# Kernel optimization log

Measured on AMD Instinct MI355X. Metric: run time of the kernel, lower is better.

## Reference

```python
import jax, jax.numpy as jnp
import numpy as np
from jax import lax

EPS = 1e-5

def _conv3x3(x, w, stride=1):
    # x: [B,C,H,W], w: [O,I,3,3]
    dn = lax.conv_dimension_numbers(x.shape, w.shape, ('NCHW', 'OIHW', 'NCHW'))
    return lax.conv_general_dilated(x, w, window_strides=(stride, stride),
                                    padding=((1, 1), (1, 1)), dimension_numbers=dn)

def _batchnorm(x, gamma, beta):
    # training-mode BN over (N,H,W) per channel
    mean = jnp.mean(x, axis=(0, 2, 3), keepdims=True)
    var = jnp.var(x, axis=(0, 2, 3), keepdims=True)
    inv = lax.rsqrt(var + EPS)
    return (x - mean) * inv * gamma[None, :, None, None] + beta[None, :, None, None]

def setup_inputs() -> dict:
    key = jax.random.key(0)
    ks = jax.random.split(key, 8)
    B, C, H, W, E = 16, 256, 64, 64, 512
    x = jax.random.normal(ks[0], (B, C, H, W), dtype=jnp.float32)
    embedding = jax.random.normal(ks[1], (B, E), dtype=jnp.float32)
    s_conv = 1.0 / np.sqrt(C * 9)
    conv1_w = jax.random.normal(ks[2], (C, C, 3, 3), dtype=jnp.float32) * s_conv
    conv2_w = jax.random.normal(ks[3], (C, C, 3, 3), dtype=jnp.float32) * s_conv
    s_g = 1.0 / np.sqrt(E)
    g1_w = jax.random.normal(ks[4], (E, C), dtype=jnp.float32) * s_g
    g1_b = jnp.zeros((C,), dtype=jnp.float32)
    g2_w = jax.random.normal(ks[5], (E, C), dtype=jnp.float32) * s_g
    g2_b = jnp.zeros((C,), dtype=jnp.float32)
    bn1_g = jnp.ones((C,), dtype=jnp.float32)
    bn1_b = jnp.zeros((C,), dtype=jnp.float32)
    bn2_g = jnp.ones((C,), dtype=jnp.float32)
    bn2_b = jnp.zeros((C,), dtype=jnp.float32)
    return {"x": x, "embedding": embedding, "conv1_w": conv1_w, "conv2_w": conv2_w,
            "g1_w": g1_w, "g1_b": g1_b, "g2_w": g2_w, "g2_b": g2_b,
            "bn1_g": bn1_g, "bn1_b": bn1_b, "bn2_g": bn2_g, "bn2_b": bn2_b}

def reference(x, embedding, conv1_w, conv2_w, g1_w, g1_b, g2_w, g2_b,
              bn1_g, bn1_b, bn2_g, bn2_b):
    identity = x
    # gate 1: per-sample per-channel gate values (softmax over channels)
    gate1 = jax.nn.softmax(embedding @ g1_w + g1_b, axis=-1)  # [B,C]
    out = _conv3x3(x, conv1_w, stride=1) * gate1[:, :, None, None]
    out = jax.nn.relu(_batchnorm(out, bn1_g, bn1_b))
    # gate 2
    gate2 = jax.nn.softmax(embedding @ g2_w + g2_b, axis=-1)  # [B,C]
    out = _conv3x3(out, conv2_w, stride=1) * gate2[:, :, None, None]
    out = _batchnorm(out, bn2_g, bn2_b)
    out = jax.nn.relu(out + identity)
    return (out, gate1, gate2)
```

## Files before the change

### kernel.cpp

```cpp
#include <hip/hip_runtime.h>

typedef __attribute__((ext_vector_type(8))) short short8;
typedef __attribute__((ext_vector_type(4))) float f32x4;

#define HP 66

__device__ __forceinline__ unsigned short f2bf(float f) {
  unsigned u = __builtin_bit_cast(unsigned, f);
  u += 0x7FFFu + ((u >> 16) & 1u);
  return (unsigned short)(u >> 16);
}
__device__ __forceinline__ float bf2f(unsigned short h) {
  return __builtin_bit_cast(float, ((unsigned)h) << 16);
}
__device__ __forceinline__ __attribute__((address_space(3))) void* to_as3(void* p) {
  return (__attribute__((address_space(3))) void*)(unsigned)(unsigned long long)p;
}
__device__ __forceinline__ const __attribute__((address_space(1))) void* to_as1(const void* p) {
  return (const __attribute__((address_space(1))) void*)(unsigned long long)p;
}

#define SB0() __builtin_amdgcn_sched_barrier(0)
#define BAR() do { SB0(); __builtin_amdgcn_s_barrier(); SB0(); } while (0)

__global__ void k_halo_zero(unsigned int* xp) {
  int p = blockIdx.x % 260;
  int b = blockIdx.x / 260;
  int h, w;
  if (p < 66)      { h = 0;  w = p; }
  else if (p < 132){ h = 65; w = p - 66; }
  else             { int q = p - 132; h = 1 + (q >> 1); w = (q & 1) * 65; }
  unsigned int* dst = xp + ((long)((b*HP + h)*HP + w) * 256) / 2;
  dst[threadIdx.x] = 0u;
  dst[threadIdx.x + 64] = 0u;
}

__global__ __launch_bounds__(256) void k_convert_x(const float* __restrict__ x,
                                                   unsigned short* __restrict__ xp) {
  __shared__ float tile[32][65];
  int blk = blockIdx.x;
  int ct = blk & 7, h = (blk >> 3) & 63, b = blk >> 9;
  int c0 = ct * 32;
  int t = threadIdx.x;
  int w = t & 63, cs = t >> 6;
#pragma unroll
  for (int i = 0; i < 8; ++i) {
    int c = cs + i * 4;
    tile[c][w] = x[(((b * 256) + c0 + c) * 64 + h) * 64 + w];
  }
  __syncthreads();
  int cl = (t & 15) * 2, w0 = t >> 4;
#pragma unroll
  for (int i = 0; i < 4; ++i) {
    int ww = w0 + i * 16;
    unsigned v = (unsigned)f2bf(tile[cl][ww]) | ((unsigned)f2bf(tile[cl + 1][ww]) << 16);
    *(unsigned*)(xp + ((long)((b*HP + h + 1)*HP + (ww + 1)) * 256 + c0 + cl)) = v;
  }
}

__global__ void k_pack_w(const float* __restrict__ w1, const float* __restrict__ w2,
                         unsigned short* __restrict__ wT1, unsigned short* __restrict__ wT2) {
  const float* w = blockIdx.y ? w2 : w1;
  unsigned short* wT = blockIdx.y ? wT2 : wT1;
  int co = blockIdx.x;
  int t = threadIdx.x;
#pragma unroll
  for (int kk = 0; kk < 9; ++kk) {
    wT[co * 2304 + kk * 256 + t] = f2bf(w[(co * 256 + t) * 9 + kk]);
  }
}

__global__ __launch_bounds__(256) void k_gates(const float* __restrict__ emb,
                                               const float* __restrict__ g1w,
                                               const float* __restrict__ g1b,
                                               const float* __restrict__ g2w,
                                               const float* __restrict__ g2b,
                                               float* __restrict__ gate1,
                                               float* __restrict__ gate2) {
  const float* gw = blockIdx.y ? g2w : g1w;
  const float* gbias = blockIdx.y ? g2b : g1b;
  float* gout = blockIdx.y ? gate2 : gate1;
  __shared__ float ebuf[512];
  __shared__ float red[8];
  int b = blockIdx.x, t = threadIdx.x;
  ebuf[t] = emb[b * 512 + t];
  ebuf[t + 256] = emb[b * 512 + t + 256];
  __syncthreads();
  float acc = gbias[t];
  for (int k = 0; k < 512; ++k) acc += ebuf[k] * gw[k * 256 + t];
  float mx = acc;
  for (int off = 32; off >= 1; off >>= 1) mx = fmaxf(mx, __shfl_xor(mx, off));
  if ((t & 63) == 0) red[t >> 6] = mx;
  __syncthreads();
  mx = fmaxf(fmaxf(red[0], red[1]), fmaxf(red[2], red[3]));
  float e = expf(acc - mx);
  float sm = e;
  for (int off = 32; off >= 1; off >>= 1) sm += __shfl_xor(sm, off);
  if ((t & 63) == 0) red[4 + (t >> 6)] = sm;
  __syncthreads();
  sm = red[4] + red[5] + red[6] + red[7];
  gout[b * 256 + t] = e / sm;
}

__global__ __launch_bounds__(512, 2) void k_conv(
    const unsigned short* __restrict__ inp,
    const unsigned short* __restrict__ wT,
    const float* __restrict__ gate,
    unsigned short* __restrict__ yout,
    float* __restrict__ partials) {
  __shared__ short As[2][256][64];
  __shared__ short Bs[2][256][64];
  __shared__ float sbuf[2][256][2];

  const int t = threadIdx.x;
  const int lane = t & 63;
  const int wid = t >> 6;
  const int wm = wid >> 2;
  const int wn = wid & 3;
  const int lr = lane & 15;
  const int hi = lane >> 4;
  const int key = lr & 7;

  const int blk = ((blockIdx.x & 7) << 5) + (blockIdx.x >> 3);
  const int b = blk >> 4;
  const int hh4 = (blk & 15) << 2;

  const int r0 = t >> 3;
  const int cdst = (t & 7) << 3;
  const int cg8 = (((t & 7) ^ ((t >> 3) & 7)) << 3);

  int aoff[4];
#pragma unroll
  for (int i = 0; i < 4; ++i)
    aoff[i] = (b * HP + hh4 + i) * HP + r0;

  auto stageA = [&](int buf, int half, int s) {
    int kk = s >> 2;
    int kh = (kk * 11) >> 5;
    int khw = kh * 66 + (kk - kh * 3);
    int ci = ((s & 3) << 6) + cg8;
    const unsigned short* g0 = inp + (long)(aoff[half * 2 + 0] + khw) * 256 + ci;
    const unsigned short* g1 = inp + (long)(aoff[half * 2 + 1] + khw) * 256 + ci;
    __builtin_amdgcn_global_load_lds(to_as1(g0), to_as3((void*)&As[buf][half * 128 + r0][cdst]), 16, 0, 0);
    __builtin_amdgcn_global_load_lds(to_as1(g1), to_as3((void*)&As[buf][half * 128 + 64 + r0][cdst]), 16, 0, 0);
  };
  auto stageB = [&](int buf, int half, int s) {
    int co0 = half * 128 + r0;
    const unsigned short* g0 = wT + (long)co0 * 2304 + s * 64 + cg8;
    const unsigned short* g1 = wT + (long)(co0 + 64) * 2304 + s * 64 + cg8;
    __builtin_amdgcn_global_load_lds(to_as1(g0), to_as3((void*)&Bs[buf][half * 128 + r0][cdst]), 16, 0, 0);
    __builtin_amdgcn_global_load_lds(to_as1(g1), to_as3((void*)&Bs[buf][half * 128 + 64 + r0][cdst]), 16, 0, 0);
  };

  f32x4 acc[8][4];
#pragma unroll
  for (int i = 0; i < 8; ++i)
#pragma unroll
    for (int j = 0; j < 4; ++j) acc[i][j] = (f32x4){0.f, 0.f, 0.f, 0.f};

  short8 afrag0[4][2], afrag1[4][2];
  short8 bfrag0[2][2], bfrag1[2][2];

#define RD_A(ARR, MH, BUF)                                                           \
  _Pragma("unroll") for (int mf = 0; mf < 4; ++mf)                                   \
    _Pragma("unroll") for (int ks = 0; ks < 2; ++ks)                                 \
      ARR[mf][ks] = *(const short8*)&As[BUF][wm * 128 + ((MH) * 4 + mf) * 16 + lr][((ks * 4 + hi) ^ key) << 3];
#define RD_B(ARR, NH, BUF)                                                           \
  _Pragma("unroll") for (int nf = 0; nf < 2; ++nf)                                   \
    _Pragma("unroll") for (int ks = 0; ks < 2; ++ks)                                 \
      ARR[nf][ks] = *(const short8*)&Bs[BUF][wn * 64 + ((NH) * 2 + nf) * 16 + lr][((ks * 4 + hi) ^ key) << 3];

#define QUADQ(AF, BF, mh, nh)                                                        \
  do {                                                                               \
    __builtin_amdgcn_s_setprio(1);                                                   \
    _Pragma("unroll") for (int ks = 0; ks < 2; ++ks)                                 \
      _Pragma("unroll") for (int mo = 0; mo < 4; ++mo)                               \
        _Pragma("unroll") for (int no = 0; no < 2; ++no)                             \
          acc[(mh) * 4 + mo][(nh) * 2 + no] = __builtin_amdgcn_mfma_f32_16x16x32_bf16( \
              AF[mo][ks], BF[no][ks], acc[(mh) * 4 + mo][(nh) * 2 + no], 0, 0, 0);   \
    __builtin_amdgcn_s_setprio(0);                                                   \
  } while (0)

  stageB(0, 1, 0); stageA(0, 0, 0); stageB(0, 0, 0); stageA(0, 1, 0);
  stageB(1, 1, 1); stageA(1, 0, 1); stageB(1, 0, 1); stageA(1, 1, 1);
  asm volatile("s_waitcnt vmcnt(8)" ::: "memory");
  BAR();
  RD_B(bfrag0, 0, 0);
  RD_A(afrag0, 0, 0);

#define KTHALF2(SEL, kt)                                                             \
  {                                                                                  \
    RD_B(bfrag1, 1, SEL);                                                            \
    RD_A(afrag1, 1, SEL);                                                            \
    if ((kt) + 2 < 36) stageB(SEL, 1, (kt) + 2);                                     \
    SB0();                                                                           \
    QUADQ(afrag0, bfrag0, 0, 0);                                                     \
    QUADQ(afrag0, bfrag1, 0, 1);                                                     \
    QUADQ(afrag1, bfrag0, 1, 0);                                                     \
    if ((kt) < 34) { asm volatile("s_waitcnt vmcnt(4)" ::: "memory"); }              \
    else           { asm volatile("s_waitcnt vmcnt(2)" ::: "memory"); }              \
    BAR();                                                                           \
    if ((kt) < 35) { RD_B(bfrag0, 0, SEL ^ 1); RD_A(afrag0, 0, SEL ^ 1); }           \
    if ((kt) + 2 < 36) { stageA(SEL, 0, (kt) + 2); stageB(SEL, 0, (kt) + 2); stageA(SEL, 1, (kt) + 2); } \
    SB0();                                                                           \
    QUADQ(afrag1, bfrag1, 1, 1);                                                     \
    if ((kt) < 34) { asm volatile("s_waitcnt vmcnt(8)" ::: "memory"); }              \
    else           { asm volatile("s_waitcnt vmcnt(0)" ::: "memory"); }              \
    BAR();                                                                           \
  }

  for (int i = 0; i < 18; ++i) {
    const int kt0 = 2 * i;
    KTHALF2(0, kt0)
    KTHALF2(1, kt0 + 1)
  }
#undef KTHALF2
#undef QUADQ
#undef RD_A
#undef RD_B

  float g[4];
#pragma unroll
  for (int nf = 0; nf < 4; ++nf) g[nf] = gate[(b << 8) + wn * 64 + nf * 16 + lr];

  float s[4] = {0, 0, 0, 0}, sq[4] = {0, 0, 0, 0};
  const int mrow0 = (blk << 8) + wm * 128 + (hi << 2);
  const int c0 = wn * 64 + lr;
#pragma unroll
  for (int mf = 0; mf < 8; ++mf)
#pragma unroll
    for (int r = 0; r < 4; ++r) {
      const int mm = mrow0 + mf * 16 + r;
#pragma unroll
      for (int nf = 0; nf < 4; ++nf) {
        float v = acc[mf][nf][r] * g[nf];
        yout[(long)mm * 256 + c0 + nf * 16] = f2bf(v);
        s[nf] += v;
        sq[nf] += v * v;
      }
    }
#pragma unroll
  for (int nf = 0; nf < 4; ++nf) {
    s[nf] += __shfl_xor(s[nf], 16);  s[nf] += __shfl_xor(s[nf], 32);
    sq[nf] += __shfl_xor(sq[nf], 16); sq[nf] += __shfl_xor(sq[nf], 32);
  }
  if (hi == 0) {
#pragma unroll
    for (int nf = 0; nf < 4; ++nf) {
      int c = wn * 64 + nf * 16 + lr;
      sbuf[wm][c][0] = s[nf];
      sbuf[wm][c][1] = sq[nf];
    }
  }
  __syncthreads();
  if (t < 256) {
    partials[((blk << 8) + t) * 2]     = sbuf[0][t][0] + sbuf[1][t][0];
    partials[((blk << 8) + t) * 2 + 1] = sbuf[0][t][1] + sbuf[1][t][1];
  }
}

__global__ __launch_bounds__(256) void k_bnfin(const float* __restrict__ partials,
                                               const float* __restrict__ gamma,
                                               const float* __restrict__ beta,
                                               float2* __restrict__ aff) {
  __shared__ float red[8];
  int c = blockIdx.x, t = threadIdx.x;
  float s = partials[(t * 256 + c) * 2];
  float sq = partials[(t * 256 + c) * 2 + 1];
  for (int off = 32; off >= 1; off >>= 1) { s += __shfl_xor(s, off); sq += __shfl_xor(sq, off); }
  if ((t & 63) == 0) { red[t >> 6] = s; red[4 + (t >> 6)] = sq; }
  __syncthreads();
  if (t == 0) {
    s = red[0] + red[1] + red[2] + red[3];
    sq = red[4] + red[5] + red[6] + red[7];
    float mean = s * (1.0f / 65536.0f);
    float var = fmaxf(sq * (1.0f / 65536.0f) - mean * mean, 0.0f);
    float inv = rsqrtf(var + 1e-5f);
    float ga = gamma[c] * inv;
    aff[c] = make_float2(ga, beta[c] - mean * ga);
  }
}

__global__ __launch_bounds__(256) void k_mid(const unsigned short* __restrict__ y1,
                                             const float2* __restrict__ aff,
                                             unsigned short* __restrict__ zp) {
  long idx = (long)blockIdx.x * 256 + threadIdx.x;
  int c0 = (int)(idx & 31) * 8;
  long pos = idx >> 5;
  int b = (int)(pos >> 12), hw = (int)(pos & 4095);
  int h = hw >> 6, w = hw & 63;
  uint4 v = *(const uint4*)(y1 + pos * 256 + c0);
  unsigned vv[4] = {v.x, v.y, v.z, v.w};
  unsigned outp[4];
#pragma unroll
  for (int j = 0; j < 4; ++j) {
    float2 aL = aff[c0 + 2 * j], aH = aff[c0 + 2 * j + 1];
    float lo = fmaxf(aL.x * bf2f((unsigned short)(vv[j] & 0xFFFF)) + aL.y, 0.f);
    float hiv = fmaxf(aH.x * bf2f((unsigned short)(vv[j] >> 16)) + aH.y, 0.f);
    outp[j] = (unsigned)f2bf(lo) | ((unsigned)f2bf(hiv) << 16);
  }
  unsigned short* dst = zp + (long)((b * HP + h + 1) * HP + w + 1) * 256 + c0;
  *(uint4*)dst = make_uint4(outp[0], outp[1], outp[2], outp[3]);
}

__global__ __launch_bounds__(256) void k_final(const unsigned short* __restrict__ y2,
                                               const float2* __restrict__ aff,
                                               const float* __restrict__ x,
                                               float* __restrict__ out) {
  __shared__ float tile[64][33];
  int blk = blockIdx.x;
  int ct = blk & 7, h = (blk >> 3) & 63, b = blk >> 9;
  int c0 = ct * 32;
  int t = threadIdx.x;
  int cl = (t & 15) * 2, w0 = t >> 4;
#pragma unroll
  for (int i = 0; i < 4; ++i) {
    int w = w0 + i * 16;
    unsigned v = *(const unsigned*)(y2 + (long)((b * 4096) + h * 64 + w) * 256 + c0 + cl);
    float2 aL = aff[c0 + cl], aH = aff[c0 + cl + 1];
    tile[w][cl] = aL.x * bf2f((unsigned short)(v & 0xFFFF)) + aL.y;
    tile[w][cl + 1] = aH.x * bf2f((unsigned short)(v >> 16)) + aH.y;
  }
  __syncthreads();
  int w = t & 63, csub = t >> 6;
#pragma unroll
  for (int j = 0; j < 8; ++j) {
    int c = c0 + csub * 8 + j;
    long o = ((long)(b * 256 + c) * 64 + h) * 64 + w;
    out[o] = fmaxf(tile[w][csub * 8 + j] + x[o], 0.f);
  }
}

extern "C" void kernel_launch(void* const* d_in, const int* in_sizes, int n_in,
                              void* d_out, int out_size, void* d_ws, size_t ws_size,
                              hipStream_t stream) {
  const float* x    = (const float*)d_in[0];
  const float* emb  = (const float*)d_in[1];
  const float* w1   = (const float*)d_in[2];
  const float* w2   = (const float*)d_in[3];
  const float* g1w  = (const float*)d_in[4];
  const float* g1b  = (const float*)d_in[5];
  const float* g2w  = (const float*)d_in[6];
  const float* g2b  = (const float*)d_in[7];
  const float* bn1g = (const float*)d_in[8];
  const float* bn1b = (const float*)d_in[9];
  const float* bn2g = (const float*)d_in[10];
  const float* bn2b = (const float*)d_in[11];

  float* out = (float*)d_out;
  float* gate1 = out + 16777216;
  float* gate2 = gate1 + 4096;

  char* ws = (char*)d_ws;
  const size_t OFF_XP  = 0;
  const size_t OFF_WT1 = 35684352;
  const size_t OFF_WT2 = OFF_WT1 + 1179648;
  const size_t OFF_Y   = OFF_WT2 + 1179648;
  const size_t OFF_PART = OFF_Y + 33554432;
  const size_t OFF_AFF1 = OFF_PART + 1048576;
  const size_t OFF_AFF2 = OFF_AFF1 + 2048;

  unsigned short* xp  = (unsigned short*)(ws + OFF_XP);
  unsigned short* wT1 = (unsigned short*)(ws + OFF_WT1);
  unsigned short* wT2 = (unsigned short*)(ws + OFF_WT2);
  unsigned short* y   = (unsigned short*)(ws + OFF_Y);
  float* part = (float*)(ws + OFF_PART);
  float2* aff1 = (float2*)(ws + OFF_AFF1);
  float2* aff2 = (float2*)(ws + OFF_AFF2);

  k_halo_zero<<<16 * 260, 64, 0, stream>>>((unsigned int*)xp);
  k_convert_x<<<8192, 256, 0, stream>>>(x, xp);
  k_pack_w<<<dim3(256, 2), 256, 0, stream>>>(w1, w2, wT1, wT2);
  k_gates<<<dim3(16, 2), 256, 0, stream>>>(emb, g1w, g1b, g2w, g2b, gate1, gate2);

  k_conv<<<256, 512, 0, stream>>>(xp, wT1, gate1, y, part);
  k_bnfin<<<256, 256, 0, stream>>>(part, bn1g, bn1b, aff1);
  k_mid<<<8192, 256, 0, stream>>>(y, aff1, xp);

  k_conv<<<256, 512, 0, stream>>>(xp, wT2, gate2, y, part);
  k_bnfin<<<256, 256, 0, stream>>>(part, bn2g, bn2b, aff2);
  k_final<<<8192, 256, 0, stream>>>(y, aff2, x, out);
}
```

Measured before the change: 226.5 us.

## Load conv weight fragments directly from global into registers, dropping LDS B staging

The weight operand B is no longer staged through shared memory. Each lane now loads its MFMA B fragments straight from global memory into double-buffered registers one k-step ahead, while only the activation tile A goes through LDS. This halves LDS footprint and removes the B LDS reads and writes. It also rewrites the pipeline schedule and waitcnt counts. The cost is more VGPR pressure and redundant global/L2 weight reads across the two wm warps, plus exposed global latency if the prefetch distance is too short.

```diff
diff --git a/kernel.cpp b/kernel.cpp
--- a/kernel.cpp
+++ b/kernel.cpp
@@ -109,7 +109,6 @@
     unsigned short* __restrict__ yout,
     float* __restrict__ partials) {
   __shared__ short As[2][256][64];
-  __shared__ short Bs[2][256][64];
   __shared__ float sbuf[2][256][2];
 
   const int t = threadIdx.x;
@@ -144,13 +143,8 @@
     __builtin_amdgcn_global_load_lds(to_as1(g0), to_as3((void*)&As[buf][half * 128 + r0][cdst]), 16, 0, 0);
     __builtin_amdgcn_global_load_lds(to_as1(g1), to_as3((void*)&As[buf][half * 128 + 64 + r0][cdst]), 16, 0, 0);
   };
-  auto stageB = [&](int buf, int half, int s) {
-    int co0 = half * 128 + r0;
-    const unsigned short* g0 = wT + (long)co0 * 2304 + s * 64 + cg8;
-    const unsigned short* g1 = wT + (long)(co0 + 64) * 2304 + s * 64 + cg8;
-    __builtin_amdgcn_global_load_lds(to_as1(g0), to_as3((void*)&Bs[buf][half * 128 + r0][cdst]), 16, 0, 0);
-    __builtin_amdgcn_global_load_lds(to_as1(g1), to_as3((void*)&Bs[buf][half * 128 + 64 + r0][cdst]), 16, 0, 0);
-  };
+
+  const unsigned short* wTq = wT + (long)(wn * 64 + lr) * 2304 + hi * 8;
 
   f32x4 acc[8][4];
 #pragma unroll
@@ -158,66 +152,85 @@
 #pragma unroll
     for (int j = 0; j < 4; ++j) acc[i][j] = (f32x4){0.f, 0.f, 0.f, 0.f};
 
-  short8 afrag0[4][2], afrag1[4][2];
-  short8 bfrag0[2][2], bfrag1[2][2];
-
-#define RD_A(ARR, MH, BUF)                                                           \
+  short8 afrag[4][2];
+  short8 bfA[4][2], bfB[4][2];
+
+#define LD_B(BF, kt)                                                                 \
+  _Pragma("unroll") for (int nf = 0; nf < 4; ++nf)                                   \
+    _Pragma("unroll") for (int ks = 0; ks < 2; ++ks)                                 \
+      BF[nf][ks] = *(const short8*)(wTq + (long)nf * 16 * 2304 + (kt) * 64 + ks * 32);
+
+#define RD_A(MH, BUF)                                                                \
   _Pragma("unroll") for (int mf = 0; mf < 4; ++mf)                                   \
     _Pragma("unroll") for (int ks = 0; ks < 2; ++ks)                                 \
-      ARR[mf][ks] = *(const short8*)&As[BUF][wm * 128 + ((MH) * 4 + mf) * 16 + lr][((ks * 4 + hi) ^ key) << 3];
-#define RD_B(ARR, NH, BUF)                                                           \
-  _Pragma("unroll") for (int nf = 0; nf < 2; ++nf)                                   \
-    _Pragma("unroll") for (int ks = 0; ks < 2; ++ks)                                 \
-      ARR[nf][ks] = *(const short8*)&Bs[BUF][wn * 64 + ((NH) * 2 + nf) * 16 + lr][((ks * 4 + hi) ^ key) << 3];
-
-#define QUADQ(AF, BF, mh, nh)                                                        \
+      afrag[mf][ks] = *(const short8*)&As[BUF][wm * 128 + ((MH) * 4 + mf) * 16 + lr][((ks * 4 + hi) ^ key) << 3];
+
+#define QUADN(BF, mh, nh)                                                            \
   do {                                                                               \
     __builtin_amdgcn_s_setprio(1);                                                   \
     _Pragma("unroll") for (int ks = 0; ks < 2; ++ks)                                 \
       _Pragma("unroll") for (int mo = 0; mo < 4; ++mo)                               \
         _Pragma("unroll") for (int no = 0; no < 2; ++no)                             \
           acc[(mh) * 4 + mo][(nh) * 2 + no] = __builtin_amdgcn_mfma_f32_16x16x32_bf16( \
-              AF[mo][ks], BF[no][ks], acc[(mh) * 4 + mo][(nh) * 2 + no], 0, 0, 0);   \
+              afrag[mo][ks], BF[(nh) * 2 + no][ks],                                  \
+              acc[(mh) * 4 + mo][(nh) * 2 + no], 0, 0, 0);                           \
     __builtin_amdgcn_s_setprio(0);                                                   \
   } while (0)
 
-  stageB(0, 1, 0); stageA(0, 0, 0); stageB(0, 0, 0); stageA(0, 1, 0);
-  stageB(1, 1, 1); stageA(1, 0, 1); stageB(1, 0, 1); stageA(1, 1, 1);
-  asm volatile("s_waitcnt vmcnt(8)" ::: "memory");
+  stageA(0, 0, 0); stageA(0, 1, 0);
+  stageA(1, 0, 1); stageA(1, 1, 1);
+  LD_B(bfA, 0);
+  asm volatile("s_waitcnt vmcnt(0)" ::: "memory");
   BAR();
-  RD_B(bfrag0, 0, 0);
-  RD_A(afrag0, 0, 0);
-
-#define KTHALF2(SEL, kt)                                                             \
+  RD_A(0, 0);
+
+#define KT_STEADY(SEL, kt, BC, BN_)                                                  \
   {                                                                                  \
-    RD_B(bfrag1, 1, SEL);                                                            \
-    RD_A(afrag1, 1, SEL);                                                            \
-    if ((kt) + 2 < 36) stageB(SEL, 1, (kt) + 2);                                     \
+    LD_B(BN_, (kt) + 1);                                                             \
     SB0();                                                                           \
-    QUADQ(afrag0, bfrag0, 0, 0);                                                     \
-    QUADQ(afrag0, bfrag1, 0, 1);                                                     \
-    QUADQ(afrag1, bfrag0, 1, 0);                                                     \
-    if ((kt) < 34) { asm volatile("s_waitcnt vmcnt(4)" ::: "memory"); }              \
-    else           { asm volatile("s_waitcnt vmcnt(2)" ::: "memory"); }              \
+    QUADN(BC, 0, 0);                                                                 \
+    QUADN(BC, 0, 1);                                                                 \
+    RD_A(1, SEL);                                                                    \
+    QUADN(BC, 1, 0);                                                                 \
+    QUADN(BC, 1, 1);                                                                 \
     BAR();                                                                           \
-    if ((kt) < 35) { RD_B(bfrag0, 0, SEL ^ 1); RD_A(afrag0, 0, SEL ^ 1); }           \
-    if ((kt) + 2 < 36) { stageA(SEL, 0, (kt) + 2); stageB(SEL, 0, (kt) + 2); stageA(SEL, 1, (kt) + 2); } \
-    SB0();                                                                           \
-    QUADQ(afrag1, bfrag1, 1, 1);                                                     \
-    if ((kt) < 34) { asm volatile("s_waitcnt vmcnt(8)" ::: "memory"); }              \
-    else           { asm volatile("s_waitcnt vmcnt(0)" ::: "memory"); }              \
+    stageA(SEL, 0, (kt) + 2); stageA(SEL, 1, (kt) + 2);                              \
+    asm volatile("s_waitcnt vmcnt(12)" ::: "memory");                                \
+    RD_A(0, SEL ^ 1);                                                                \
+    asm volatile("s_waitcnt vmcnt(4)" ::: "memory");                                 \
     BAR();                                                                           \
   }
 
-  for (int i = 0; i < 18; ++i) {
+  for (int i = 0; i < 17; ++i) {
     const int kt0 = 2 * i;
-    KTHALF2(0, kt0)
-    KTHALF2(1, kt0 + 1)
-  }
-#undef KTHALF2
-#undef QUADQ
+    KT_STEADY(0, kt0, bfA, bfB)
+    KT_STEADY(1, kt0 + 1, bfB, bfA)
+  }
+  {
+    LD_B(bfB, 35);
+    SB0();
+    QUADN(bfA, 0, 0);
+    QUADN(bfA, 0, 1);
+    RD_A(1, 0);
+    QUADN(bfA, 1, 0);
+    QUADN(bfA, 1, 1);
+    BAR();
+    asm volatile("s_waitcnt vmcnt(8)" ::: "memory");
+    RD_A(0, 1);
+    asm volatile("s_waitcnt vmcnt(0)" ::: "memory");
+    BAR();
+  }
+  {
+    QUADN(bfB, 0, 0);
+    QUADN(bfB, 0, 1);
+    RD_A(1, 1);
+    QUADN(bfB, 1, 0);
+    QUADN(bfB, 1, 1);
+  }
+#undef KT_STEADY
+#undef QUADN
 #undef RD_A
-#undef RD_B
+#undef LD_B
 
   float g[4];
 #pragma unroll
@@ -244,6 +257,7 @@
     s[nf] += __shfl_xor(s[nf], 16);  s[nf] += __shfl_xor(s[nf], 32);
     sq[nf] += __shfl_xor(sq[nf], 16); sq[nf] += __shfl_xor(sq[nf], 32);
   }
+  __syncthreads();
   if (hi == 0) {
 #pragma unroll
     for (int nf = 0; nf < 4; ++nf) {
```

New measurement: 293.0 us. 29.3% more time.

## Merge prep kernels into one launch and stage conv output through LDS

Applied to the files above, without the earlier changes.

Folds the halo-zero, input conversion, weight packing and gate softmax kernels into one k_prep launch that dispatches on block index, cutting three kernel launches and their gaps. In the conv epilogue, the gated bf16 results are first written into the reused LDS pool and then stored to global memory as coalesced 16-byte rows, replacing scattered 2-byte stores. LDS is now a single aliased pool. The A/B tile area is reused for the output only after the barrier that ends the main loop, which relies on that barrier being in place.

```diff
diff --git a/kernel.cpp b/kernel.cpp
--- a/kernel.cpp
+++ b/kernel.cpp
@@ -23,83 +23,78 @@
 #define SB0() __builtin_amdgcn_sched_barrier(0)
 #define BAR() do { SB0(); __builtin_amdgcn_s_barrier(); SB0(); } while (0)
 
-__global__ void k_halo_zero(unsigned int* xp) {
-  int p = blockIdx.x % 260;
-  int b = blockIdx.x / 260;
-  int h, w;
-  if (p < 66)      { h = 0;  w = p; }
-  else if (p < 132){ h = 65; w = p - 66; }
-  else             { int q = p - 132; h = 1 + (q >> 1); w = (q & 1) * 65; }
-  unsigned int* dst = xp + ((long)((b*HP + h)*HP + w) * 256) / 2;
-  dst[threadIdx.x] = 0u;
-  dst[threadIdx.x + 64] = 0u;
-}
-
-__global__ __launch_bounds__(256) void k_convert_x(const float* __restrict__ x,
-                                                   unsigned short* __restrict__ xp) {
+__global__ __launch_bounds__(256) void k_prep(
+    const float* __restrict__ x, unsigned short* __restrict__ xp,
+    const float* __restrict__ w1, const float* __restrict__ w2,
+    unsigned short* __restrict__ wT1, unsigned short* __restrict__ wT2,
+    const float* __restrict__ emb,
+    const float* __restrict__ g1w, const float* __restrict__ g1b,
+    const float* __restrict__ g2w, const float* __restrict__ g2b,
+    float* __restrict__ gate1, float* __restrict__ gate2) {
   __shared__ float tile[32][65];
-  int blk = blockIdx.x;
-  int ct = blk & 7, h = (blk >> 3) & 63, b = blk >> 9;
-  int c0 = ct * 32;
-  int t = threadIdx.x;
-  int w = t & 63, cs = t >> 6;
-#pragma unroll
-  for (int i = 0; i < 8; ++i) {
-    int c = cs + i * 4;
-    tile[c][w] = x[(((b * 256) + c0 + c) * 64 + h) * 64 + w];
-  }
-  __syncthreads();
-  int cl = (t & 15) * 2, w0 = t >> 4;
-#pragma unroll
-  for (int i = 0; i < 4; ++i) {
-    int ww = w0 + i * 16;
-    unsigned v = (unsigned)f2bf(tile[cl][ww]) | ((unsigned)f2bf(tile[cl + 1][ww]) << 16);
-    *(unsigned*)(xp + ((long)((b*HP + h + 1)*HP + (ww + 1)) * 256 + c0 + cl)) = v;
-  }
-}
-
-__global__ void k_pack_w(const float* __restrict__ w1, const float* __restrict__ w2,
-                         unsigned short* __restrict__ wT1, unsigned short* __restrict__ wT2) {
-  const float* w = blockIdx.y ? w2 : w1;
-  unsigned short* wT = blockIdx.y ? wT2 : wT1;
-  int co = blockIdx.x;
-  int t = threadIdx.x;
-#pragma unroll
-  for (int kk = 0; kk < 9; ++kk) {
-    wT[co * 2304 + kk * 256 + t] = f2bf(w[(co * 256 + t) * 9 + kk]);
-  }
-}
-
-__global__ __launch_bounds__(256) void k_gates(const float* __restrict__ emb,
-                                               const float* __restrict__ g1w,
-                                               const float* __restrict__ g1b,
-                                               const float* __restrict__ g2w,
-                                               const float* __restrict__ g2b,
-                                               float* __restrict__ gate1,
-                                               float* __restrict__ gate2) {
-  const float* gw = blockIdx.y ? g2w : g1w;
-  const float* gbias = blockIdx.y ? g2b : g1b;
-  float* gout = blockIdx.y ? gate2 : gate1;
   __shared__ float ebuf[512];
   __shared__ float red[8];
-  int b = blockIdx.x, t = threadIdx.x;
-  ebuf[t] = emb[b * 512 + t];
-  ebuf[t + 256] = emb[b * 512 + t + 256];
-  __syncthreads();
-  float acc = gbias[t];
-  for (int k = 0; k < 512; ++k) acc += ebuf[k] * gw[k * 256 + t];
-  float mx = acc;
-  for (int off = 32; off >= 1; off >>= 1) mx = fmaxf(mx, __shfl_xor(mx, off));
-  if ((t & 63) == 0) red[t >> 6] = mx;
-  __syncthreads();
-  mx = fmaxf(fmaxf(red[0], red[1]), fmaxf(red[2], red[3]));
-  float e = expf(acc - mx);
-  float sm = e;
-  for (int off = 32; off >= 1; off >>= 1) sm += __shfl_xor(sm, off);
-  if ((t & 63) == 0) red[4 + (t >> 6)] = sm;
-  __syncthreads();
-  sm = red[4] + red[5] + red[6] + red[7];
-  gout[b * 256 + t] = e / sm;
+  const int blk = blockIdx.x;
+  const int t = threadIdx.x;
+
+  if (blk < 8192) {
+    int ct = blk & 7, h = (blk >> 3) & 63, b = blk >> 9;
+    int c0 = ct * 32;
+    int w = t & 63, cs = t >> 6;
+#pragma unroll
+    for (int i = 0; i < 8; ++i) {
+      int c = cs + i * 4;
+      tile[c][w] = x[(((b * 256) + c0 + c) * 64 + h) * 64 + w];
+    }
+    __syncthreads();
+    int cl = (t & 15) * 2, w0 = t >> 4;
+#pragma unroll
+    for (int i = 0; i < 4; ++i) {
+      int ww = w0 + i * 16;
+      unsigned v = (unsigned)f2bf(tile[cl][ww]) | ((unsigned)f2bf(tile[cl + 1][ww]) << 16);
+      *(unsigned*)(xp + ((long)((b*HP + h + 1)*HP + (ww + 1)) * 256 + c0 + cl)) = v;
+    }
+  } else if (blk < 10272) {
+    unsigned u = (unsigned)(blk - 8192) * 256 + t;
+    unsigned p_idx = u >> 7, word = u & 127;
+    int img = p_idx / 260, p = p_idx % 260;
+    int h, w;
+    if (p < 66)      { h = 0;  w = p; }
+    else if (p < 132){ h = 65; w = p - 66; }
+    else             { int q = p - 132; h = 1 + (q >> 1); w = (q & 1) * 65; }
+    ((unsigned*)xp)[((long)((img*HP + h)*HP + w) * 256) / 2 + word] = 0u;
+  } else if (blk < 10784) {
+    int idx = blk - 10272;
+    const float* w = (idx >> 8) ? w2 : w1;
+    unsigned short* wT = (idx >> 8) ? wT2 : wT1;
+    int co = idx & 255;
+#pragma unroll
+    for (int kk = 0; kk < 9; ++kk)
+      wT[co * 2304 + kk * 256 + t] = f2bf(w[(co * 256 + t) * 9 + kk]);
+  } else {
+    int idx = blk - 10784;
+    int b = idx & 15;
+    const float* gw = (idx >> 4) ? g2w : g1w;
+    const float* gbias = (idx >> 4) ? g2b : g1b;
+    float* gout = (idx >> 4) ? gate2 : gate1;
+    ebuf[t] = emb[b * 512 + t];
+    ebuf[t + 256] = emb[b * 512 + t + 256];
+    __syncthreads();
+    float acc = gbias[t];
+    for (int k = 0; k < 512; ++k) acc += ebuf[k] * gw[k * 256 + t];
+    float mx = acc;
+    for (int off = 32; off >= 1; off >>= 1) mx = fmaxf(mx, __shfl_xor(mx, off));
+    if ((t & 63) == 0) red[t >> 6] = mx;
+    __syncthreads();
+    mx = fmaxf(fmaxf(red[0], red[1]), fmaxf(red[2], red[3]));
+    float e = expf(acc - mx);
+    float sm = e;
+    for (int off = 32; off >= 1; off >>= 1) sm += __shfl_xor(sm, off);
+    if ((t & 63) == 0) red[4 + (t >> 6)] = sm;
+    __syncthreads();
+    sm = red[4] + red[5] + red[6] + red[7];
+    gout[b * 256 + t] = e / sm;
+  }
 }
 
 __global__ __launch_bounds__(512, 2) void k_conv(
@@ -108,9 +103,10 @@
     const float* __restrict__ gate,
     unsigned short* __restrict__ yout,
     float* __restrict__ partials) {
-  __shared__ short As[2][256][64];
-  __shared__ short Bs[2][256][64];
-  __shared__ float sbuf[2][256][2];
+  __shared__ __align__(16) char pool[135168];
+  auto As = reinterpret_cast<short(*)[256][64]>(pool);
+  auto Bs = reinterpret_cast<short(*)[256][64]>(pool + 65536);
+  auto sbuf = reinterpret_cast<float(*)[256][2]>(pool + 131072);
 
   const int t = threadIdx.x;
   const int lane = t & 63;
@@ -223,22 +219,22 @@
 #pragma unroll
   for (int nf = 0; nf < 4; ++nf) g[nf] = gate[(b << 8) + wn * 64 + nf * 16 + lr];
 
+  auto LZ = reinterpret_cast<unsigned short(*)[256]>(pool);
   float s[4] = {0, 0, 0, 0}, sq[4] = {0, 0, 0, 0};
-  const int mrow0 = (blk << 8) + wm * 128 + (hi << 2);
-  const int c0 = wn * 64 + lr;
-#pragma unroll
-  for (int mf = 0; mf < 8; ++mf)
+#pragma unroll
+  for (int mf = 0; mf < 8; ++mf) {
+    const int rowb = wm * 128 + mf * 16 + (hi << 2);
 #pragma unroll
     for (int r = 0; r < 4; ++r) {
-      const int mm = mrow0 + mf * 16 + r;
 #pragma unroll
       for (int nf = 0; nf < 4; ++nf) {
         float v = acc[mf][nf][r] * g[nf];
-        yout[(long)mm * 256 + c0 + nf * 16] = f2bf(v);
+        LZ[rowb + r][wn * 64 + nf * 16 + lr] = f2bf(v);
         s[nf] += v;
         sq[nf] += v * v;
       }
     }
+  }
 #pragma unroll
   for (int nf = 0; nf < 4; ++nf) {
     s[nf] += __shfl_xor(s[nf], 16);  s[nf] += __shfl_xor(s[nf], 32);
@@ -253,6 +249,12 @@
     }
   }
   __syncthreads();
+#pragma unroll
+  for (int it = 0; it < 16; ++it) {
+    const int row = it * 16 + (t >> 5);
+    *(uint4*)(yout + (long)(blk * 256 + row) * 256 + (t & 31) * 8) =
+        *(const uint4*)&LZ[row][(t & 31) * 8];
+  }
   if (t < 256) {
     partials[((blk << 8) + t) * 2]     = sbuf[0][t][0] + sbuf[1][t][0];
     partials[((blk << 8) + t) * 2 + 1] = sbuf[0][t][1] + sbuf[1][t][1];
@@ -368,10 +370,8 @@
   float2* aff1 = (float2*)(ws + OFF_AFF1);
   float2* aff2 = (float2*)(ws + OFF_AFF2);
 
-  k_halo_zero<<<16 * 260, 64, 0, stream>>>((unsigned int*)xp);
-  k_convert_x<<<8192, 256, 0, stream>>>(x, xp);
-  k_pack_w<<<dim3(256, 2), 256, 0, stream>>>(w1, w2, wT1, wT2);
-  k_gates<<<dim3(16, 2), 256, 0, stream>>>(emb, g1w, g1b, g2w, g2b, gate1, gate2);
+  k_prep<<<10816, 256, 0, stream>>>(x, xp, w1, w2, wT1, wT2, emb,
+                                    g1w, g1b, g2w, g2b, gate1, gate2);
 
   k_conv<<<256, 512, 0, stream>>>(xp, wT1, gate1, y, part);
   k_bnfin<<<256, 256, 0, stream>>>(part, bn1g, bn1b, aff1);
```

New measurement: 247.8 us. 1.09x slower.
